# Performance work log

Hardware: AMD Instinct MI355X
Metric: run time of the kernel (lower is better)

The kernel has to match this reference:

```python
import jax, jax.numpy as jnp
import numpy as np

M = 0.5
S = 64.0
LS_EPS = 0.0
COS_M = float(np.cos(M))
SIN_M = float(np.sin(M))
THRESHOLD = float(np.cos(np.pi - M))
MM = float(np.sin(np.pi - M) * M)
N_CLASSES = 100000


def setup_inputs() -> dict:
    key = jax.random.key(0)
    k1, k2, k3 = jax.random.split(key, 3)
    embeddings = jax.random.normal(k1, (1024, 512), dtype=jnp.float32)
    kernel = jax.random.normal(k2, (512, N_CLASSES), dtype=jnp.float32) * 0.01
    t = jnp.zeros((1,), dtype=jnp.float32)
    label = jax.random.randint(k3, (1024,), 0, N_CLASSES, dtype=jnp.int64)
    return {"embeddings": embeddings, "kernel": kernel, "t": t, "label": label}


def reference(embeddings, kernel, t, label):
    # l2-normalize embeddings over feature axis, kernel over input axis
    emb = embeddings / jnp.linalg.norm(embeddings, axis=1, keepdims=True)
    kn = kernel / jnp.linalg.norm(kernel, axis=0, keepdims=True)
    cos_theta = jnp.clip(emb @ kn, -1.0, 1.0)  # [N, C]
    n = embeddings.shape[0]
    rows = jnp.arange(n)
    target_logit = cos_theta[rows, label][:, None]  # [N, 1]
    sin_theta = jnp.sqrt(1.0 - target_logit ** 2)
    cos_theta_m = target_logit * COS_M - sin_theta * SIN_M  # [N, 1]
    mask = cos_theta > cos_theta_m  # hard examples (broadcast per row)
    final_target_logit = jnp.where(target_logit > THRESHOLD,
                                   cos_theta_m, target_logit - MM)
    # running-mean buffer update (no-grad in original)
    t_new = jax.lax.stop_gradient(target_logit.mean() * 0.01 + 0.99 * t[0])
    cos_theta = jnp.where(mask, cos_theta * (t_new + cos_theta), cos_theta)
    cos_theta = cos_theta.at[rows, label].set(final_target_logit[:, 0])
    if LS_EPS > 0:
        cos_theta = (1 - LS_EPS) * cos_theta + LS_EPS / N_CLASSES
    return cos_theta * S
```

## Files before the change

### kernel.cpp

```cpp
#include <hip/hip_runtime.h>

typedef unsigned short u16;
typedef unsigned int u32;
typedef __attribute__((ext_vector_type(8))) short bf16x8;
typedef __attribute__((ext_vector_type(4))) float f32x4;

#define KDIM   512
#define NROWS  1024
#define NCLS   100000
#define CPAD   100096

#define COS_M_C   0.8775825618903728f
#define SIN_M_C   0.4794255386042030f
#define THRESH_C  (-0.8775825618903728f)
#define MM_C      0.2397127693021015f
#define S_C       64.0f

__device__ __forceinline__ u16 f2bf(float f) {
    u32 x = __float_as_uint(f);
    x += 0x7fffu + ((x >> 16) & 1u);
    return (u16)(x >> 16);
}
__device__ __forceinline__ float bf2f(u16 u) {
    return __uint_as_float(((u32)u) << 16);
}

__device__ __forceinline__ void gld16(const void* g, void* l) {
    __builtin_amdgcn_global_load_lds(
        (const __attribute__((address_space(1))) void*)g,
        (__attribute__((address_space(3))) void*)l, 16, 0, 0);
}

__global__ __launch_bounds__(64)
void norm_emb_k(const float* __restrict__ emb, float* __restrict__ Af,
                u16* __restrict__ Aw) {
    const int i = blockIdx.x, l = threadIdx.x;
    const float* e = emb + i * KDIM;
    float4 v0 = *(const float4*)(e + l * 4);
    float4 v1 = *(const float4*)(e + 256 + l * 4);
    float s = v0.x*v0.x + v0.y*v0.y + v0.z*v0.z + v0.w*v0.w
            + v1.x*v1.x + v1.y*v1.y + v1.z*v1.z + v1.w*v1.w;
    #pragma unroll
    for (int o = 1; o < 64; o <<= 1) s += __shfl_xor(s, o);
    float inv = rsqrtf(s);
    float4 n0 = make_float4(v0.x*inv, v0.y*inv, v0.z*inv, v0.w*inv);
    float4 n1 = make_float4(v1.x*inv, v1.y*inv, v1.z*inv, v1.w*inv);
    *(float4*)(Af + i*KDIM + l*4)       = n0;
    *(float4*)(Af + i*KDIM + 256 + l*4) = n1;
    ushort4 p0 = { f2bf(n0.x), f2bf(n0.y), f2bf(n0.z), f2bf(n0.w) };
    ushort4 p1 = { f2bf(n1.x), f2bf(n1.y), f2bf(n1.z), f2bf(n1.w) };
    *(ushort4*)(Aw + i*KDIM + l*4)       = p0;
    *(ushort4*)(Aw + i*KDIM + 256 + l*4) = p1;
}

__global__ __launch_bounds__(128)
void transpose_norm_k(const float* __restrict__ Kg, u16* __restrict__ Bn,
                      float* __restrict__ kinv) {
    __shared__ float Ls[32 * 132];
    const int t  = threadIdx.x;
    const int jb = blockIdx.x * 128;
    const int j  = jb + t;
    float acc = 0.f;
    for (int kc = 0; kc < 16; ++kc) {
        #pragma unroll
        for (int it = 0; it < 8; ++it) {
            int fid  = it * 128 + t;
            int r    = fid >> 5;
            int c4   = (fid & 31) * 4;
            int gcol = jb + c4;
            float4 v;
            if (gcol + 3 < NCLS) {
                v = *(const float4*)(Kg + (kc*32 + r) * NCLS + gcol);
            } else {
                v.x = (gcol + 0 < NCLS) ? Kg[(kc*32 + r)*NCLS + gcol + 0] : 0.f;
                v.y = (gcol + 1 < NCLS) ? Kg[(kc*32 + r)*NCLS + gcol + 1] : 0.f;
                v.z = (gcol + 2 < NCLS) ? Kg[(kc*32 + r)*NCLS + gcol + 2] : 0.f;
                v.w = (gcol + 3 < NCLS) ? Kg[(kc*32 + r)*NCLS + gcol + 3] : 0.f;
            }
            *(float4*)(Ls + r * 132 + c4) = v;
        }
        __syncthreads();
        #pragma unroll
        for (int g = 0; g < 4; ++g) {
            u16 u[8];
            #pragma unroll
            for (int e = 0; e < 8; ++e) {
                float v = Ls[(g*8 + e) * 132 + t];
                acc += v * v;
                u[e] = f2bf(v);
            }
            uint4 w;
            w.x = (u32)u[0] | ((u32)u[1] << 16);
            w.y = (u32)u[2] | ((u32)u[3] << 16);
            w.z = (u32)u[4] | ((u32)u[5] << 16);
            w.w = (u32)u[6] | ((u32)u[7] << 16);
            *(uint4*)(Bn + (size_t)j * KDIM + kc*32 + g*8) = w;
        }
        __syncthreads();
    }
    kinv[j] = rsqrtf(fmaxf(acc, 1e-30f));
}

__global__ __launch_bounds__(64)
void target_k(const float* __restrict__ Af, const u16* __restrict__ Bn,
              const float* __restrict__ kinv, const int* __restrict__ label,
              float* __restrict__ tgt, float* __restrict__ ctm,
              float* __restrict__ fin) {
    const int i = blockIdx.x, l = threadIdx.x;
    const int lab = label[i];
    const float* a = Af + i * KDIM + l * 8;
    float4 a0 = *(const float4*)a;
    float4 a1 = *(const float4*)(a + 4);
    uint4 bv = *(const uint4*)(Bn + (size_t)lab * KDIM + l * 8);
    float d = a0.x * bf2f((u16)(bv.x & 0xffff)) + a0.y * bf2f((u16)(bv.x >> 16))
            + a0.z * bf2f((u16)(bv.y & 0xffff)) + a0.w * bf2f((u16)(bv.y >> 16))
            + a1.x * bf2f((u16)(bv.z & 0xffff)) + a1.y * bf2f((u16)(bv.z >> 16))
            + a1.z * bf2f((u16)(bv.w & 0xffff)) + a1.w * bf2f((u16)(bv.w >> 16));
    #pragma unroll
    for (int o = 1; o < 64; o <<= 1) d += __shfl_xor(d, o);
    if (l == 0) {
        float c = d * kinv[lab];
        c = fminf(fmaxf(c, -1.f), 1.f);
        tgt[i] = c;
        float sn = sqrtf(fmaxf(1.f - c*c, 0.f));
        float cm = c * COS_M_C - sn * SIN_M_C;
        ctm[i] = cm;
        fin[i] = (c > THRESH_C) ? cm : (c - MM_C);
    }
}

__global__ __launch_bounds__(256)
void tnew_k(const float* __restrict__ tgt, const float* __restrict__ tin,
            float* __restrict__ tnw) {
    __shared__ float red[256];
    const int t = threadIdx.x;
    float s = tgt[t] + tgt[t + 256] + tgt[t + 512] + tgt[t + 768];
    red[t] = s;
    __syncthreads();
    for (int o = 128; o > 0; o >>= 1) {
        if (t < o) red[t] += red[t + o];
        __syncthreads();
    }
    if (t == 0) tnw[0] = red[0] * (0.01f / 1024.f) + 0.99f * tin[0];
}

__global__ __launch_bounds__(256)
void gemm_k(const u16* __restrict__ A, const u16* __restrict__ B,
            const float* __restrict__ kinv, const float* __restrict__ ctm,
            const float* __restrict__ fin, const int* __restrict__ label,
            const float* __restrict__ tnwp, float* __restrict__ out) {
    __shared__ __align__(16) u16 As[128 * 32];
    __shared__ __align__(16) u16 Bs[128 * 32];
    const int tid  = threadIdx.x;
    const int wave = tid >> 6, lane = tid & 63;
    const int m0 = blockIdx.x * 128;
    const int j0 = blockIdx.y * 128;
    const int wr = (wave >> 1) * 64;
    const int wc = (wave & 1) * 64;

    f32x4 acc[4][4] = {};

    const int o0 = wave * 1024 + lane * 16;
    const int o1 = o0 + 4096;
    const int rA0 = o0 >> 6, cA0 = (o0 & 63) >> 1;
    const int rA1 = o1 >> 6, cA1 = (o1 & 63) >> 1;
    const u16* gA0 = A + (m0 + rA0) * KDIM + cA0;
    const u16* gA1 = A + (m0 + rA1) * KDIM + cA1;
    const u16* gB0 = B + (size_t)(j0 + rA0) * KDIM + cA0;
    const u16* gB1 = B + (size_t)(j0 + rA1) * KDIM + cA1;
    u16* lA0 = As + (o0 >> 1);
    u16* lA1 = As + (o1 >> 1);
    u16* lB0 = Bs + (o0 >> 1);
    u16* lB1 = Bs + (o1 >> 1);

    const char* aBase = (const char*)As + ((wr + (lane & 15)) * 64) + ((lane >> 4) * 16);
    const char* bBase = (const char*)Bs + ((wc + (lane & 15)) * 64) + ((lane >> 4) * 16);

    for (int ks = 0; ks < KDIM / 32; ++ks) {
        const int k0 = ks * 32;
        gld16(gA0 + k0, lA0);
        gld16(gA1 + k0, lA1);
        gld16(gB0 + k0, lB0);
        gld16(gB1 + k0, lB1);
        __syncthreads();

        bf16x8 af[4], bfr[4];
        #pragma unroll
        for (int m = 0; m < 4; ++m)
            af[m] = *(const bf16x8*)(aBase + m * 16 * 64);
        #pragma unroll
        for (int n = 0; n < 4; ++n)
            bfr[n] = *(const bf16x8*)(bBase + n * 16 * 64);
        #pragma unroll
        for (int m = 0; m < 4; ++m)
            #pragma unroll
            for (int n = 0; n < 4; ++n)
                acc[m][n] = __builtin_amdgcn_mfma_f32_16x16x32_bf16(
                                af[m], bfr[n], acc[m][n], 0, 0, 0);
        __syncthreads();
    }

    const float tnew = *tnwp;
    const int colbase = j0 + wc + (lane & 15);
    float kv[4];
    int cols[4];
    #pragma unroll
    for (int n = 0; n < 4; ++n) {
        cols[n] = colbase + n * 16;
        kv[n] = (cols[n] < NCLS) ? kinv[cols[n]] : 0.f;
    }
    #pragma unroll
    for (int m = 0; m < 4; ++m) {
        const int rb = m0 + wr + m * 16 + (lane >> 4) * 4;
        #pragma unroll
        for (int r = 0; r < 4; ++r) {
            const int row = rb + r;
            const int lab = label[row];
            const float ct = ctm[row];
            const float fv = fin[row];
            float* orow = out + (size_t)row * NCLS;
            #pragma unroll
            for (int n = 0; n < 4; ++n) {
                float c = acc[m][n][r] * kv[n];
                c = fminf(fmaxf(c, -1.f), 1.f);
                float v = (c > ct) ? c * (tnew + c) : c;
                v = (cols[n] == lab) ? fv : v;
                if (cols[n] < NCLS)
                    __builtin_nontemporal_store(v * S_C, orow + cols[n]);
            }
        }
    }
}

extern "C" void kernel_launch(void* const* d_in, const int* in_sizes, int n_in,
                              void* d_out, int out_size, void* d_ws, size_t ws_size,
                              hipStream_t stream) {
    const float* emb = (const float*)d_in[0];
    const float* Kg  = (const float*)d_in[1];
    const float* tin = (const float*)d_in[2];
    const int*   lab = (const int*)d_in[3];
    float* out = (float*)d_out;

    char* w = (char*)d_ws;
    u16*   Bn   = (u16*)w;
    u16*   Aw   = (u16*)(w + 102498304);
    float* Af   = (float*)(w + 103546880);
    float* kinv = (float*)(w + 105644032);
    float* tgt  = (float*)(w + 106044416);
    float* ctmv = (float*)(w + 106048512);
    float* finv = (float*)(w + 106052608);
    float* tnw  = (float*)(w + 106056704);

    norm_emb_k<<<NROWS, 64, 0, stream>>>(emb, Af, Aw);
    transpose_norm_k<<<CPAD / 128, 128, 0, stream>>>(Kg, Bn, kinv);
    target_k<<<NROWS, 64, 0, stream>>>(Af, Bn, kinv, lab, tgt, ctmv, finv);
    tnew_k<<<1, 256, 0, stream>>>(tgt, tin, tnw);
    gemm_k<<<dim3(NROWS / 128, CPAD / 128), 256, 0, stream>>>(
        Aw, Bn, kinv, ctmv, finv, lab, tnw, out);
}
```

Before: 381.8 us.

## Tile-major B layout, double-buffered GEMM pipeline, XCD-aware block swizzle

Stores the normalized bf16 kernel matrix in 128-column strips with contiguous 32-wide K chunks, so each GEMM tile load reads one contiguous 8 KB block. The target lookup is updated to the same layout. The GEMM now double-buffers LDS, prefetching the next K slice while MFMAs run on the current one, using explicit waitcnt and barriers in place of __syncthreads. It also remaps the 1D grid so that blocks sharing a column strip land on the same XCD for L2 reuse, and it replaces nontemporal output stores with normal stores. The manual vmcnt accounting depends on the exact number of loads issued per stage.

```diff
diff --git a/kernel.cpp b/kernel.cpp
--- a/kernel.cpp
+++ b/kernel.cpp
@@ -9,6 +9,8 @@
 #define NROWS  1024
 #define NCLS   100000
 #define CPAD   100096
+#define NSTRIP 782
+#define NMT    8
 
 #define COS_M_C   0.8775825618903728f
 #define SIN_M_C   0.4794255386042030f
@@ -60,6 +62,7 @@
     const int t  = threadIdx.x;
     const int jb = blockIdx.x * 128;
     const int j  = jb + t;
+    u16* bstrip = Bn + (size_t)blockIdx.x * 65536;
     float acc = 0.f;
     for (int kc = 0; kc < 16; ++kc) {
         #pragma unroll
@@ -94,7 +97,7 @@
             w.y = (u32)u[2] | ((u32)u[3] << 16);
             w.z = (u32)u[4] | ((u32)u[5] << 16);
             w.w = (u32)u[6] | ((u32)u[7] << 16);
-            *(uint4*)(Bn + (size_t)j * KDIM + kc*32 + g*8) = w;
+            *(uint4*)(bstrip + kc*4096 + t*32 + g*8) = w;
         }
         __syncthreads();
     }
@@ -111,7 +114,8 @@
     const float* a = Af + i * KDIM + l * 8;
     float4 a0 = *(const float4*)a;
     float4 a1 = *(const float4*)(a + 4);
-    uint4 bv = *(const uint4*)(Bn + (size_t)lab * KDIM + l * 8);
+    uint4 bv = *(const uint4*)(Bn + (size_t)(lab >> 7) * 65536
+                               + (l >> 2) * 4096 + (lab & 127) * 32 + (l & 3) * 8);
     float d = a0.x * bf2f((u16)(bv.x & 0xffff)) + a0.y * bf2f((u16)(bv.x >> 16))
             + a0.z * bf2f((u16)(bv.y & 0xffff)) + a0.w * bf2f((u16)(bv.y >> 16))
             + a1.x * bf2f((u16)(bv.z & 0xffff)) + a1.y * bf2f((u16)(bv.z >> 16))
@@ -149,56 +153,79 @@
             const float* __restrict__ kinv, const float* __restrict__ ctm,
             const float* __restrict__ fin, const int* __restrict__ label,
             const float* __restrict__ tnwp, float* __restrict__ out) {
-    __shared__ __align__(16) u16 As[128 * 32];
-    __shared__ __align__(16) u16 Bs[128 * 32];
+    __shared__ __align__(16) u16 As[2][4096];
+    __shared__ __align__(16) u16 Bs[2][4096];
     const int tid  = threadIdx.x;
     const int wave = tid >> 6, lane = tid & 63;
-    const int m0 = blockIdx.x * 128;
-    const int j0 = blockIdx.y * 128;
+
+    const int L  = blockIdx.x;
+    const int w  = (L & 7) * NSTRIP + (L >> 3);
+    const int mt = w & 7;
+    const int cs = w >> 3;
+    const int m0 = mt * 128;
+    const int j0 = cs * 128;
     const int wr = (wave >> 1) * 64;
     const int wc = (wave & 1) * 64;
 
     f32x4 acc[4][4] = {};
 
-    const int o0 = wave * 1024 + lane * 16;
+    const int o0 = tid * 16;
     const int o1 = o0 + 4096;
     const int rA0 = o0 >> 6, cA0 = (o0 & 63) >> 1;
     const int rA1 = o1 >> 6, cA1 = (o1 & 63) >> 1;
     const u16* gA0 = A + (m0 + rA0) * KDIM + cA0;
     const u16* gA1 = A + (m0 + rA1) * KDIM + cA1;
-    const u16* gB0 = B + (size_t)(j0 + rA0) * KDIM + cA0;
-    const u16* gB1 = B + (size_t)(j0 + rA1) * KDIM + cA1;
-    u16* lA0 = As + (o0 >> 1);
-    u16* lA1 = As + (o1 >> 1);
-    u16* lB0 = Bs + (o0 >> 1);
-    u16* lB1 = Bs + (o1 >> 1);
-
-    const char* aBase = (const char*)As + ((wr + (lane & 15)) * 64) + ((lane >> 4) * 16);
-    const char* bBase = (const char*)Bs + ((wc + (lane & 15)) * 64) + ((lane >> 4) * 16);
-
-    for (int ks = 0; ks < KDIM / 32; ++ks) {
-        const int k0 = ks * 32;
-        gld16(gA0 + k0, lA0);
-        gld16(gA1 + k0, lA1);
-        gld16(gB0 + k0, lB0);
-        gld16(gB1 + k0, lB1);
-        __syncthreads();
-
+    const u16* gB0 = B + (size_t)cs * 65536 + (o0 >> 1);
+    const u16* gB1 = gB0 + 2048;
+    const int lOff0 = o0 >> 1;
+    const int lOff1 = lOff0 + 2048;
+
+    const int aOff = (wr + (lane & 15)) * 64 + (lane >> 4) * 16;
+    const int bOff = (wc + (lane & 15)) * 64 + (lane >> 4) * 16;
+
+#define STAGE(b, ks)                                            \
+    do {                                                        \
+        gld16(gA0 + (ks) * 32, &As[b][lOff0]);                  \
+        gld16(gA1 + (ks) * 32, &As[b][lOff1]);                  \
+        gld16(gB0 + (ks) * 4096, &Bs[b][lOff0]);                \
+        gld16(gB1 + (ks) * 4096, &Bs[b][lOff1]);                \
+    } while (0)
+
+    STAGE(0, 0);
+    int cur = 0;
+    #pragma unroll 2
+    for (int ks = 0; ks < 16; ++ks) {
+        if (ks < 15) {
+            STAGE(cur ^ 1, ks + 1);
+            asm volatile("s_waitcnt vmcnt(4)" ::: "memory");
+        } else {
+            asm volatile("s_waitcnt vmcnt(0)" ::: "memory");
+        }
+        __builtin_amdgcn_s_barrier();
+        __builtin_amdgcn_sched_barrier(0);
+
+        const char* aB = (const char*)As[cur] + aOff;
+        const char* bB = (const char*)Bs[cur] + bOff;
         bf16x8 af[4], bfr[4];
         #pragma unroll
         for (int m = 0; m < 4; ++m)
-            af[m] = *(const bf16x8*)(aBase + m * 16 * 64);
+            af[m] = *(const bf16x8*)(aB + m * 1024);
         #pragma unroll
         for (int n = 0; n < 4; ++n)
-            bfr[n] = *(const bf16x8*)(bBase + n * 16 * 64);
+            bfr[n] = *(const bf16x8*)(bB + n * 1024);
         #pragma unroll
         for (int m = 0; m < 4; ++m)
             #pragma unroll
             for (int n = 0; n < 4; ++n)
                 acc[m][n] = __builtin_amdgcn_mfma_f32_16x16x32_bf16(
                                 af[m], bfr[n], acc[m][n], 0, 0, 0);
-        __syncthreads();
-    }
+
+        asm volatile("s_waitcnt lgkmcnt(0)" ::: "memory");
+        __builtin_amdgcn_s_barrier();
+        __builtin_amdgcn_sched_barrier(0);
+        cur ^= 1;
+    }
+#undef STAGE
 
     const float tnew = *tnwp;
     const int colbase = j0 + wc + (lane & 15);
@@ -226,7 +253,7 @@
                 float v = (c > ct) ? c * (tnew + c) : c;
                 v = (cols[n] == lab) ? fv : v;
                 if (cols[n] < NCLS)
-                    __builtin_nontemporal_store(v * S_C, orow + cols[n]);
+                    orow[cols[n]] = v * S_C;
             }
         }
     }
@@ -252,9 +279,9 @@
     float* tnw  = (float*)(w + 106056704);
 
     norm_emb_k<<<NROWS, 64, 0, stream>>>(emb, Af, Aw);
-    transpose_norm_k<<<CPAD / 128, 128, 0, stream>>>(Kg, Bn, kinv);
+    transpose_norm_k<<<NSTRIP, 128, 0, stream>>>(Kg, Bn, kinv);
     target_k<<<NROWS, 64, 0, stream>>>(Af, Bn, kinv, lab, tgt, ctmv, finv);
     tnew_k<<<1, 256, 0, stream>>>(tgt, tin, tnw);
-    gemm_k<<<dim3(NROWS / 128, CPAD / 128), 256, 0, stream>>>(
+    gemm_k<<<NSTRIP * NMT, 256, 0, stream>>>(
         Aw, Bn, kinv, ctmv, finv, lab, tnw, out);
 }
```

Result: slower. 415.3 us (+8.8%).
